# Kernel optimization log

Hardware: AMD Instinct MI355X
Metric: run time of the kernel (lower is better)

The kernel has to match this reference:

```python
import jax, jax.numpy as jnp
import numpy as np

B, FEAT, SPD_H, CTRL_H, N_CMD = 32768, 512, 128, 256, 4


def _p(key, shape, fan_in):
    # torch nn.Linear default init: U(-1/sqrt(fan_in), 1/sqrt(fan_in))
    lim = 1.0 / np.sqrt(fan_in)
    return jax.random.uniform(key, shape, jnp.float32, -lim, lim)


def setup_inputs() -> dict:
    key = jax.random.key(0)
    ks = iter(jax.random.split(key, 32))
    inp = {
        "feat": jax.random.normal(next(ks), (B, FEAT), jnp.float32),
        "speed": jax.random.uniform(next(ks), (B,), jnp.float32),
        "command": jax.random.randint(next(ks), (B,), 0, N_CMD, jnp.int32),
        "ms_w1": _p(next(ks), (1, SPD_H), 1), "ms_b1": _p(next(ks), (SPD_H,), 1),
        "ms_w2": _p(next(ks), (SPD_H, SPD_H), SPD_H), "ms_b2": _p(next(ks), (SPD_H,), SPD_H),
        "ms_w3": _p(next(ks), (SPD_H, SPD_H), SPD_H), "ms_b3": _p(next(ks), (SPD_H,), SPD_H),
        # speed_pred_module: 512 -> 256 -> 256 -> 1
        "sp_w1": _p(next(ks), (FEAT, CTRL_H), FEAT), "sp_b1": _p(next(ks), (CTRL_H,), FEAT),
        "sp_w2": _p(next(ks), (CTRL_H, CTRL_H), CTRL_H), "sp_b2": _p(next(ks), (CTRL_H,), CTRL_H),
        "sp_w3": _p(next(ks), (CTRL_H, 1), CTRL_H), "sp_b3": _p(next(ks), (1,), CTRL_H),
        # join_module: Linear(640, 512)
        "join_w": _p(next(ks), (FEAT + SPD_H, FEAT), FEAT + SPD_H),
        "join_b": _p(next(ks), (FEAT,), FEAT + SPD_H),
        # 4 control heads: 512 -> 256 -> 256 -> 3 (stacked on expert axis e)
        "ctrl_w1": _p(next(ks), (N_CMD, FEAT, CTRL_H), FEAT), "ctrl_b1": _p(next(ks), (N_CMD, CTRL_H), FEAT),
        "ctrl_w2": _p(next(ks), (N_CMD, CTRL_H, CTRL_H), CTRL_H), "ctrl_b2": _p(next(ks), (N_CMD, CTRL_H), CTRL_H),
        "ctrl_w3": _p(next(ks), (N_CMD, CTRL_H, 3), CTRL_H), "ctrl_b3": _p(next(ks), (N_CMD, 3), CTRL_H),
    }
    return inp


def _mlp(x, w1, b1, w2, b2, w3, b3):
    # FullyConnectedNet: Linear, ReLU, Linear, Dropout(p=0 -> noop), ReLU, Linear
    h = jax.nn.relu(x @ w1 + b1)
    h = jax.nn.relu(h @ w2 + b2)
    return h @ w3 + b3


def reference(feat, speed, command,
              ms_w1, ms_b1, ms_w2, ms_b2, ms_w3, ms_b3,
              sp_w1, sp_b1, sp_w2, sp_b2, sp_w3, sp_b3,
              join_w, join_b,
              ctrl_w1, ctrl_b1, ctrl_w2, ctrl_b2, ctrl_w3, ctrl_b3):
    v = _mlp(speed[:, None], ms_w1, ms_b1, ms_w2, ms_b2, ms_w3, ms_b3)      # [B,128]
    joined = jnp.concatenate([feat, v], axis=1) @ join_w + join_b           # [B,512]
    v_p = _mlp(feat, sp_w1, sp_b1, sp_w2, sp_b2, sp_w3, sp_b3)              # [B,1]
    # command-indexed dispatch: compute all 4 heads densely, then select per sample
    h1 = jax.nn.relu(jnp.einsum('bd,edh->beh', joined, ctrl_w1) + ctrl_b1)  # [B,4,256]
    h2 = jax.nn.relu(jnp.einsum('beh,ehk->bek', h1, ctrl_w2) + ctrl_b2)     # [B,4,256]
    act_all = jnp.einsum('bek,eko->beo', h2, ctrl_w3) + ctrl_b3             # [B,4,3]
    action = jnp.take_along_axis(act_all, command[:, None, None].astype(jnp.int32), axis=1)[:, 0]  # [B,3]
    throttle = jax.nn.sigmoid(action[:, 0])
    steering = jnp.tanh(action[:, 1])
    brake = jax.nn.sigmoid(action[:, 2])
    return v_p, throttle, brake, steering
```

## Files before the change

kernel.cpp:

```cpp
#include <hip/hip_runtime.h>
#include <hip/hip_bf16.h>
#include <stdint.h>
#include <math.h>

#define BB 32768
#define FEAT 512
#define SPD_H 128
#define CTRL_H 256
#define NCMD 4

typedef __attribute__((ext_vector_type(8))) short bf16x8;
typedef __attribute__((ext_vector_type(4))) float f32x4;

__device__ __forceinline__ unsigned short f2bf(float f) {
  union { float f; uint32_t u; } v; v.f = f;
  uint32_t u = v.u;
  return (unsigned short)((u + 0x7fffu + ((u >> 16) & 1u)) >> 16);
}

__device__ __forceinline__ void async16(const unsigned short* g, unsigned short* l) {
  __builtin_amdgcn_global_load_lds(
      (const __attribute__((address_space(1))) unsigned int*)g,
      (__attribute__((address_space(3))) unsigned int*)l, 16, 0, 0);
}

__device__ __forceinline__ void gemm128(
    const unsigned short* __restrict__ A, int lda,
    const int* __restrict__ perm, int m_start, int m_cnt,
    const unsigned short* __restrict__ W, const float* __restrict__ bi,
    unsigned short* __restrict__ C, int ldc, int relu, int K, int mt, int nt) {
  extern __shared__ __align__(16) unsigned char dynsm[];
  unsigned short* As = (unsigned short*)dynsm;
  unsigned short* Bs = As + 128 * 32;

  const int m0 = mt * 128;
  if (m0 >= m_cnt) return;
  const int n0 = nt * 128;
  const int t = threadIdx.x;
  const int w = t >> 6, lane = t & 63;
  const int wm = w & 1, wn = w >> 1;

  f32x4 acc[4][4];
#pragma unroll
  for (int i = 0; i < 4; ++i)
#pragma unroll
    for (int j = 0; j < 4; ++j)
#pragma unroll
      for (int r = 0; r < 4; ++r) acc[i][j][r] = 0.f;

  const int fr = lane & 15;
  const int fk = (lane >> 4) * 8;

  const unsigned short* agp[2]; const unsigned short* bgp[2];
  unsigned short* al[2]; unsigned short* bl[2];
#pragma unroll
  for (int it = 0; it < 2; ++it) {
    int row = w * 32 + it * 16 + (lane >> 2);
    int seg8 = (lane & 3) * 8;
    int rl = m0 + row;
    if (rl >= m_cnt) rl = m_cnt - 1;
    int grow = perm ? perm[m_start + rl] : (m_start + rl);
    agp[it] = A + (size_t)grow * lda + seg8;
    bgp[it] = W + (size_t)(n0 + row) * K + seg8;
    al[it] = As + (w * 32 + it * 16) * 32;
    bl[it] = Bs + (w * 32 + it * 16) * 32;
  }

  for (int k0 = 0; k0 < K; k0 += 32) {
#pragma unroll
    for (int it = 0; it < 2; ++it) {
      async16(agp[it] + k0, al[it]);
      async16(bgp[it] + k0, bl[it]);
    }
    __syncthreads();
    bf16x8 af[4], bfv[4];
#pragma unroll
    for (int i = 0; i < 4; ++i)
      af[i] = *(const bf16x8*)(As + (wm * 64 + i * 16 + fr) * 32 + fk);
#pragma unroll
    for (int j = 0; j < 4; ++j)
      bfv[j] = *(const bf16x8*)(Bs + (wn * 64 + j * 16 + fr) * 32 + fk);
#pragma unroll
    for (int i = 0; i < 4; ++i)
#pragma unroll
      for (int j = 0; j < 4; ++j)
        acc[i][j] = __builtin_amdgcn_mfma_f32_16x16x32_bf16(af[i], bfv[j], acc[i][j], 0, 0, 0);
    __syncthreads();
  }

  const int rquad = (lane >> 4) * 4;
  const int cidx = lane & 15;

  float bv[4];
#pragma unroll
  for (int j = 0; j < 4; ++j) bv[j] = bi ? bi[n0 + wn * 64 + j * 16 + cidx] : 0.f;

  unsigned short (*bscr)[136] = (unsigned short(*)[136])dynsm;
#pragma unroll
  for (int c = 0; c < 4; ++c) {
    if (wm == (c >> 1)) {
#pragma unroll
      for (int j = 0; j < 4; ++j) {
#pragma unroll
        for (int ii = 0; ii < 2; ++ii) {
          int i = 2 * (c & 1) + ii;
          int lr = ii * 16 + rquad;
#pragma unroll
          for (int r = 0; r < 4; ++r) {
            float v = acc[i][j][r] + bv[j];
            if (relu) v = fmaxf(v, 0.f);
            bscr[lr + r][wn * 64 + j * 16 + cidx] = f2bf(v);
          }
        }
      }
    }
    __syncthreads();
#pragma unroll
    for (int q = 0; q < 2; ++q) {
      int sg = t + 256 * q;
      int lr = sg >> 4, cs = (sg & 15) * 8;
      int grow = m0 + c * 32 + lr;
      if (grow < m_cnt)
        *(bf16x8*)(C + (size_t)(m_start + grow) * ldc + (n0 + cs)) =
            *(const bf16x8*)(&bscr[lr][cs]);
    }
    __syncthreads();
  }
}

struct WSeg { const float* src; unsigned short* dst; int K; int N; int ldd; };
struct PrepArgs {
  WSeg s[12];
  int start[13];
  const float* join_w; unsigned short* wjbf;
  const float* feat; unsigned short* ajoin;
  const int* cmd; int* wavecnt;
  const float* join_b; const float* ctrl_w1; const float* ctrl_b1; float* b_f;
};
__launch_bounds__(256)
__global__ void k_prep(PrepArgs a) {
  int bx = blockIdx.x, t = threadIdx.x;
  if (bx < 16384) {
    int idx = bx * 256 + t;
    int i = idx >> 7;
    int j4 = (idx & 127) << 2;
    float4 f = *(const float4*)(a.feat + (size_t)i * FEAT + j4);
    ushort4 o;
    o.x = f2bf(f.x); o.y = f2bf(f.y); o.z = f2bf(f.z); o.w = f2bf(f.w);
    *(ushort4*)(a.ajoin + (size_t)i * 640 + j4) = o;
    return;
  }
  int rel = bx - 16384;
  if (rel < 320) {
    int idx = rel * 256 + t;
    float4 f = *(const float4*)(a.join_w + (size_t)idx * 4);
    ushort4 o;
    o.x = f2bf(f.x); o.y = f2bf(f.y); o.z = f2bf(f.z); o.w = f2bf(f.w);
    *(ushort4*)(a.wjbf + (size_t)idx * 4) = o;
    return;
  }
  rel -= 320;
  if (rel < a.start[12]) {
    __shared__ float tb[32][33];
    int si = 0;
    while (rel >= a.start[si + 1]) ++si;
    WSeg sg = a.s[si];
    int tile = rel - a.start[si];
    int tkx = sg.K >> 5;
    int tn = tile / tkx;
    int tk = tile - tn * tkx;
    int k0 = tk * 32, n0 = tn * 32;
    int tx = t & 31, ty = t >> 5;
#pragma unroll
    for (int j = 0; j < 4; ++j)
      tb[ty + j * 8][tx] = sg.src[(size_t)(k0 + ty + j * 8) * sg.N + n0 + tx];
    __syncthreads();
#pragma unroll
    for (int j = 0; j < 4; ++j)
      sg.dst[(size_t)(n0 + ty + j * 8) * sg.ldd + k0 + tx] = f2bf(tb[tx][ty + j * 8]);
    return;
  }
  rel -= a.start[12];
  if (rel < 128) {
    int i = rel * 256 + t;
    int c = a.cmd[i];
    int wid = i >> 6;
    int lane = t & 63;
#pragma unroll
    for (int cv = 0; cv < NCMD; ++cv) {
      unsigned long long m = __ballot(c == cv);
      if (lane == 0) a.wavecnt[cv * 512 + wid] = __popcll(m);
    }
    return;
  }
  int e = rel - 128;
  float s = a.ctrl_b1[e * 256 + t];
  const float* w = a.ctrl_w1 + (size_t)e * 512 * 256 + t;
  for (int m = 0; m < 512; ++m) s = fmaf(a.join_b[m], w[(size_t)m * 256], s);
  a.b_f[e * 256 + t] = s;
}

struct MidArgs {
  const int* cmd; const int* wavecnt; int* perm; int* offs;
  const unsigned short* c_w1t; const unsigned short* wjbf; unsigned short* wf_t;
  const float* speed;
  const float* ms_w1; const float* ms_b1;
  const unsigned short* ms_w2t; const float* ms_b2;
  const unsigned short* ms_w3t; const float* ms_b3;
  unsigned short* ajoin;
};
__launch_bounds__(256)
__global__ void k_mid(MidArgs a) {
  int b = blockIdx.x, t = threadIdx.x;
  if (b >= 168) {
    extern __shared__ __align__(16) unsigned char dynsm[];
    unsigned short (*hw)[136] = (unsigned short(*)[136])dynsm;
    unsigned short* BsM = (unsigned short*)(dynsm + 128 * 136 * 2);
    const int m0 = (b - 168) * 128;
    const int w = t >> 6, lane = t & 63;
    const int wm = w & 1, wn = w >> 1;
    const int fr = lane & 15, fk = (lane >> 4) * 8;
    const int rquad = (lane >> 4) * 4, cidx = lane & 15;
    {
      int r = t >> 1, half = t & 1;
      float s = a.speed[m0 + r];
#pragma unroll
      for (int c0 = 0; c0 < 64; c0 += 4) {
        int c = half * 64 + c0;
        float4 wv = *(const float4*)(a.ms_w1 + c);
        float4 bv = *(const float4*)(a.ms_b1 + c);
        hw[r][c + 0] = f2bf(fmaxf(fmaf(s, wv.x, bv.x), 0.f));
        hw[r][c + 1] = f2bf(fmaxf(fmaf(s, wv.y, bv.y), 0.f));
        hw[r][c + 2] = f2bf(fmaxf(fmaf(s, wv.z, bv.z), 0.f));
        hw[r][c + 3] = f2bf(fmaxf(fmaf(s, wv.w, bv.w), 0.f));
      }
    }
    __syncthreads();
    for (int layer = 0; layer < 2; ++layer) {
      const unsigned short* Wt = layer ? a.ms_w3t : a.ms_w2t;
      const float* bb = layer ? a.ms_b3 : a.ms_b2;
      f32x4 acc[4][4];
#pragma unroll
      for (int i = 0; i < 4; ++i)
#pragma unroll
        for (int j = 0; j < 4; ++j)
#pragma unroll
          for (int r = 0; r < 4; ++r) acc[i][j][r] = 0.f;
      for (int k0 = 0; k0 < 128; k0 += 32) {
#pragma unroll
        for (int it = 0; it < 2; ++it) {
          int row = w * 32 + it * 16 + (lane >> 2);
          async16(Wt + (size_t)row * 128 + k0 + (lane & 3) * 8,
                  BsM + (w * 32 + it * 16) * 32);
        }
        __syncthreads();
        bf16x8 af[4], bfv[4];
#pragma unroll
        for (int i = 0; i < 4; ++i)
          af[i] = *(const bf16x8*)(&hw[wm * 64 + i * 16 + fr][k0 + fk]);
#pragma unroll
        for (int j = 0; j < 4; ++j)
          bfv[j] = *(const bf16x8*)(BsM + (wn * 64 + j * 16 + fr) * 32 + fk);
#pragma unroll
        for (int i = 0; i < 4; ++i)
#pragma unroll
          for (int j = 0; j < 4; ++j)
            acc[i][j] = __builtin_amdgcn_mfma_f32_16x16x32_bf16(af[i], bfv[j], acc[i][j], 0, 0, 0);
        __syncthreads();
      }
#pragma unroll
      for (int j = 0; j < 4; ++j) {
        int col = wn * 64 + j * 16 + cidx;
        float bv = bb[col];
#pragma unroll
        for (int i = 0; i < 4; ++i) {
          int row = wm * 64 + i * 16 + rquad;
#pragma unroll
          for (int r = 0; r < 4; ++r) {
            float v = acc[i][j][r] + bv;
            if (layer == 0) v = fmaxf(v, 0.f);
            hw[row + r][col] = f2bf(v);
          }
        }
      }
      __syncthreads();
    }
    {
      int r = t >> 1, half = t & 1;
#pragma unroll
      for (int c8 = 0; c8 < 8; ++c8)
        *(bf16x8*)(a.ajoin + (size_t)(m0 + r) * 640 + 512 + half * 64 + c8 * 8) =
            *(const bf16x8*)(&hw[r][half * 64 + c8 * 8]);
    }
    return;
  }
  if (b >= 128) {
    int idx = b - 128;
    int mt = idx & 7, nt = idx >> 3;
    gemm128(a.c_w1t, 512, nullptr, 0, 1024, a.wjbf, nullptr, a.wf_t, 640, 0, 512, mt, nt);
    return;
  }
  __shared__ int pf[NCMD][4];
  __shared__ int tot[NCMD];
  int c = t >> 6, lane = t & 63;
  int v[8]; int s = 0;
#pragma unroll
  for (int q = 0; q < 8; ++q) { v[q] = a.wavecnt[c * 512 + lane * 8 + q]; s += v[q]; }
  int p = s;
#pragma unroll
  for (int m = 1; m < 64; m <<= 1) { int o = __shfl_up(p, m, 64); if (lane >= m) p += o; }
  int excl = p - s;
  if (lane == 63) tot[c] = p;
  if (lane == ((4 * b) >> 3)) {
    int base_off = (4 * b) & 7;
    int run = excl;
#pragma unroll
    for (int q = 0; q < 8; ++q) {
      if (q >= base_off && q < base_off + 4) pf[c][q - base_off] = run;
      run += v[q];
    }
  }
  __syncthreads();
  int soffs[NCMD + 1];
  soffs[0] = 0;
#pragma unroll
  for (int e = 0; e < NCMD; ++e) soffs[e + 1] = soffs[e] + tot[e];
  if (b == 0 && t == 0)
    for (int e = 0; e <= NCMD; ++e) a.offs[e] = soffs[e];
  int i = b * 256 + t;
  int mc = a.cmd[i];
  int lwid = t >> 6;
  int rank = 0, base = 0;
#pragma unroll
  for (int cv = 0; cv < NCMD; ++cv) {
    unsigned long long m = __ballot(mc == cv);
    if (mc == cv) {
      rank = __popcll(m & ((1ull << lane) - 1ull));
      base = soffs[cv] + pf[cv][lwid];
    }
  }
  a.perm[base + rank] = i;
}

struct MainArgs {
  const unsigned short* ajoin;
  const unsigned short* wf_t; const float* b_f;
  const unsigned short* sp_w1t; const float* sp_b1;
  unsigned short* ch1; unsigned short* sph1p;
  const int* perm; const int* seg;
};
__launch_bounds__(256)
__global__ void k_main(MainArgs a) {
  const int e = blockIdx.z;
  const int gid = blockIdx.x;
  const int mt = gid & 255, nt = gid >> 8;
  int ms = a.seg[e], mc = a.seg[e + 1] - ms;
  if (nt < 2) {
    gemm128(a.ajoin, 640, a.perm, ms, mc, a.wf_t + (size_t)e * 256 * 640,
            a.b_f + e * 256, a.ch1, 256, 1, 640, mt, nt);
  } else {
    gemm128(a.ajoin, 640, a.perm, ms, mc, a.sp_w1t, a.sp_b1,
            a.sph1p, 256, 1, 512, mt, nt - 2);
  }
}

struct VArgs {
  const unsigned short* A_s; const unsigned short* A_c;
  const unsigned short* W_s; const unsigned short* W_c;
  const float* b_s; const float* b_c;
  const float* w3_s; const float* b3_s;
  const float* w3_c; const float* b3_c;
  const int* perm; const int* seg;
  float* out;
};
__launch_bounds__(256)
__global__ void k_vgemm(VArgs a) {
  __shared__ unsigned short As[64 * 32];
  __shared__ unsigned short Bs[256 * 32];
  const int z = blockIdx.z;
  const unsigned short* A; const unsigned short* W; const float* bi;
  int m_start, m_cnt;
  if (z == 4) { A = a.A_s; W = a.W_s; bi = a.b_s; m_start = 0; m_cnt = BB; }
  else {
    A = a.A_c; W = a.W_c + (size_t)z * 65536; bi = a.b_c + z * 256;
    m_start = a.seg[z]; m_cnt = a.seg[z + 1] - m_start;
  }
  const int m0 = blockIdx.x * 64;
  if (m0 >= m_cnt) return;
  const int t = threadIdx.x, w = t >> 6, lane = t & 63;
  const int fr = lane & 15, fk = (lane >> 4) * 8;

  f32x4 acc[16];
#pragma unroll
  for (int j = 0; j < 16; ++j)
#pragma unroll
    for (int r = 0; r < 4; ++r) acc[j][r] = 0.f;

  int arow = m0 + w * 16 + (lane >> 2);
  if (arow >= m_cnt) arow = m_cnt - 1;
  const unsigned short* ap = A + (size_t)(m_start + arow) * 256 + (lane & 3) * 8;
  unsigned short* al = As + (w * 16) * 32;
  const unsigned short* bp[4]; unsigned short* bl[4];
#pragma unroll
  for (int it = 0; it < 4; ++it) {
    int brow = w * 64 + it * 16 + (lane >> 2);
    bp[it] = W + (size_t)brow * 256 + (lane & 3) * 8;
    bl[it] = Bs + (w * 64 + it * 16) * 32;
  }

  for (int k0 = 0; k0 < 256; k0 += 32) {
    async16(ap + k0, al);
#pragma unroll
    for (int it = 0; it < 4; ++it) async16(bp[it] + k0, bl[it]);
    __syncthreads();
    bf16x8 af = *(const bf16x8*)(As + (w * 16 + fr) * 32 + fk);
#pragma unroll
    for (int j = 0; j < 16; ++j) {
      bf16x8 bfv = *(const bf16x8*)(Bs + (j * 16 + fr) * 32 + fk);
      acc[j] = __builtin_amdgcn_mfma_f32_16x16x32_bf16(af, bfv, acc[j], 0, 0, 0);
    }
    __syncthreads();
  }

  const int rquad = (lane >> 4) * 4;
  float bcol[16];
#pragma unroll
  for (int j = 0; j < 16; ++j) bcol[j] = bi[j * 16 + fr];

  if (z == 4) {
    float aw[16];
#pragma unroll
    for (int j = 0; j < 16; ++j) aw[j] = a.w3_s[j * 16 + fr];
#pragma unroll
    for (int r = 0; r < 4; ++r) {
      float s = 0.f;
#pragma unroll
      for (int j = 0; j < 16; ++j)
        s = fmaf(fmaxf(acc[j][r] + bcol[j], 0.f), aw[j], s);
      s += __shfl_xor(s, 1, 64);
      s += __shfl_xor(s, 2, 64);
      s += __shfl_xor(s, 4, 64);
      s += __shfl_xor(s, 8, 64);
      int row = m0 + w * 16 + rquad + r;
      if (fr == 0 && row < m_cnt)
        a.out[a.perm[row]] = s + a.b3_s[0];
    }
  } else {
    float aw0[16], aw1[16], aw2[16];
#pragma unroll
    for (int j = 0; j < 16; ++j) {
      const float* wp = a.w3_c + (size_t)z * 768 + (j * 16 + fr) * 3;
      aw0[j] = wp[0]; aw1[j] = wp[1]; aw2[j] = wp[2];
    }
#pragma unroll
    for (int r = 0; r < 4; ++r) {
      float s0 = 0.f, s1 = 0.f, s2 = 0.f;
#pragma unroll
      for (int j = 0; j < 16; ++j) {
        float v = fmaxf(acc[j][r] + bcol[j], 0.f);
        s0 = fmaf(v, aw0[j], s0);
        s1 = fmaf(v, aw1[j], s1);
        s2 = fmaf(v, aw2[j], s2);
      }
#pragma unroll
      for (int m = 1; m <= 8; m <<= 1) {
        s0 += __shfl_xor(s0, m, 64);
        s1 += __shfl_xor(s1, m, 64);
        s2 += __shfl_xor(s2, m, 64);
      }
      int row = m0 + w * 16 + rquad + r;
      if (fr == 0 && row < m_cnt) {
        int orig = a.perm[m_start + row];
        float a0 = s0 + a.b3_c[z * 3 + 0];
        float a1 = s1 + a.b3_c[z * 3 + 1];
        float a2 = s2 + a.b3_c[z * 3 + 2];
        a.out[BB + orig]     = 1.f / (1.f + __expf(-a0));
        a.out[2 * BB + orig] = 1.f / (1.f + __expf(-a2));
        a.out[3 * BB + orig] = tanhf(a1);
      }
    }
  }
}

static inline size_t align256(size_t x) { return (x + 255) & ~(size_t)255; }

extern "C" void kernel_launch(void* const* d_in, const int* in_sizes, int n_in,
                              void* d_out, int out_size, void* d_ws, size_t ws_size,
                              hipStream_t stream) {
  const float* feat   = (const float*)d_in[0];
  const float* speed  = (const float*)d_in[1];
  const int*   command= (const int*)d_in[2];
  const float* ms_w1  = (const float*)d_in[3];
  const float* ms_b1  = (const float*)d_in[4];
  const float* ms_w2  = (const float*)d_in[5];
  const float* ms_b2  = (const float*)d_in[6];
  const float* ms_w3  = (const float*)d_in[7];
  const float* ms_b3  = (const float*)d_in[8];
  const float* sp_w1  = (const float*)d_in[9];
  const float* sp_b1  = (const float*)d_in[10];
  const float* sp_w2  = (const float*)d_in[11];
  const float* sp_b2  = (const float*)d_in[12];
  const float* sp_w3  = (const float*)d_in[13];
  const float* sp_b3  = (const float*)d_in[14];
  const float* join_w = (const float*)d_in[15];
  const float* join_b = (const float*)d_in[16];
  const float* ctrl_w1= (const float*)d_in[17];
  const float* ctrl_b1= (const float*)d_in[18];
  const float* ctrl_w2= (const float*)d_in[19];
  const float* ctrl_b2= (const float*)d_in[20];
  const float* ctrl_w3= (const float*)d_in[21];
  const float* ctrl_b3= (const float*)d_in[22];
  float* out = (float*)d_out;

  char* ws = (char*)d_ws;
  size_t off = 0;
  auto alloc = [&](size_t bytes) -> char* { char* p = ws + off; off = align256(off + bytes); return p; };

  unsigned short* ajoin  = (unsigned short*)alloc((size_t)BB * 640 * 2);
  unsigned short* sph1p  = (unsigned short*)alloc((size_t)BB * 256 * 2);
  unsigned short* ch1    = (unsigned short*)alloc((size_t)BB * 256 * 2);
  unsigned short* wtp    = (unsigned short*)alloc(1998848ull * 2);
  int* perm    = (int*)alloc((size_t)BB * 4);
  int* cnt     = (int*)alloc(64);
  int* wavecnt = (int*)alloc(4 * 512 * 4);
  float* b_f   = (float*)alloc(4 * 256 * 4);

  unsigned short* sp_w1t = wtp;
  unsigned short* sp_w2t = wtp + 131072;
  unsigned short* ms_w2t = wtp + 196608;
  unsigned short* ms_w3t = wtp + 212992;
  unsigned short* c_w1t  = wtp + 229376;
  unsigned short* c_w2t  = wtp + 753664;
  unsigned short* wjbf   = wtp + 1015808;
  unsigned short* wf_t   = wtp + 1343488;

  PrepArgs P;
  P.s[0] = { sp_w1, sp_w1t, 512, 256, 512 };
  P.s[1] = { sp_w2, sp_w2t, 256, 256, 256 };
  P.s[2] = { ms_w2, ms_w2t, 128, 128, 128 };
  P.s[3] = { ms_w3, ms_w3t, 128, 128, 128 };
  for (int e = 0; e < 4; ++e) P.s[4 + e] = { ctrl_w1 + (size_t)e * 512 * 256, c_w1t + (size_t)e * 131072, 512, 256, 512 };
  for (int e = 0; e < 4; ++e) P.s[8 + e] = { ctrl_w2 + (size_t)e * 256 * 256, c_w2t + (size_t)e * 65536, 256, 256, 256 };
  P.start[0] = 0;
  for (int i = 0; i < 12; ++i)
    P.start[i + 1] = P.start[i] + (P.s[i].K >> 5) * (P.s[i].N >> 5);
  P.join_w = join_w; P.wjbf = wjbf;
  P.feat = feat; P.ajoin = ajoin;
  P.cmd = command; P.wavecnt = wavecnt;
  P.join_b = join_b; P.ctrl_w1 = ctrl_w1; P.ctrl_b1 = ctrl_b1; P.b_f = b_f;
  int prep_blocks = 16384 + 320 + P.start[12] + 128 + 4;

  k_prep<<<prep_blocks, 256, 0, stream>>>(P);

  MidArgs Mi;
  Mi.cmd = command; Mi.wavecnt = wavecnt; Mi.perm = perm; Mi.offs = cnt + 4;
  Mi.c_w1t = c_w1t; Mi.wjbf = wjbf; Mi.wf_t = wf_t;
  Mi.speed = speed;
  Mi.ms_w1 = ms_w1; Mi.ms_b1 = ms_b1;
  Mi.ms_w2t = ms_w2t; Mi.ms_b2 = ms_b2;
  Mi.ms_w3t = ms_w3t; Mi.ms_b3 = ms_b3;
  Mi.ajoin = ajoin;
  k_mid<<<168 + 256, 256, 128 * 136 * 2 + 128 * 32 * 2, stream>>>(Mi);

  MainArgs Ma;
  Ma.ajoin = ajoin; Ma.wf_t = wf_t; Ma.b_f = b_f;
  Ma.sp_w1t = sp_w1t; Ma.sp_b1 = sp_b1;
  Ma.ch1 = ch1; Ma.sph1p = sph1p;
  Ma.perm = perm; Ma.seg = cnt + 4;
  k_main<<<dim3(1024, 1, 4), 256, 128 * 32 * 2 * 2, stream>>>(Ma);

  VArgs V;
  V.A_s = sph1p; V.A_c = ch1; V.W_s = sp_w2t; V.W_c = c_w2t;
  V.b_s = sp_b2; V.b_c = ctrl_b2;
  V.w3_s = sp_w3; V.b3_s = sp_b3; V.w3_c = ctrl_w3; V.b3_c = ctrl_b3;
  V.perm = perm; V.seg = cnt + 4; V.out = out;
  k_vgemm<<<dim3(512, 1, 5), 256, 0, stream>>>(V);
}
```

Before: 232.8 us.

## Triple-buffer GEMM loads, compact expert tile grid, split bias fold, unpermute speed head

The 128x128 GEMM now uses three LDS stages with asynchronous global-to-LDS prefetch two k-steps ahead and explicit vmcnt waits, and k_vgemm double-buffers its loads. This hides load latency behind the MFMA work. k_main launches a compact list of per-expert 128-row tiles built in k_mid instead of 1024x4 mostly idle blocks, and the speed-prediction GEMM runs on unpermuted rows so its output write no longer goes through perm. The join-bias fold into the ctrl_w1 bias is split across 32 blocks with partial sums that are reduced in k_mid. The cost is more LDS per block (48 KB), which may lower occupancy.

```diff
diff --git a/kernel.cpp b/kernel.cpp
--- a/kernel.cpp
+++ b/kernel.cpp
@@ -24,14 +24,14 @@
       (__attribute__((address_space(3))) unsigned int*)l, 16, 0, 0);
 }
 
-__device__ __forceinline__ void gemm128(
+__device__ __forceinline__ void gemm128_db(
     const unsigned short* __restrict__ A, int lda,
     const int* __restrict__ perm, int m_start, int m_cnt,
     const unsigned short* __restrict__ W, const float* __restrict__ bi,
     unsigned short* __restrict__ C, int ldc, int relu, int K, int mt, int nt) {
   extern __shared__ __align__(16) unsigned char dynsm[];
   unsigned short* As = (unsigned short*)dynsm;
-  unsigned short* Bs = As + 128 * 32;
+  unsigned short* Bs = As + 3 * 4096;
 
   const int m0 = mt * 128;
   if (m0 >= m_cnt) return;
@@ -66,26 +66,49 @@
     bl[it] = Bs + (w * 32 + it * 16) * 32;
   }
 
-  for (int k0 = 0; k0 < K; k0 += 32) {
+  const int nk = K >> 5;
+#pragma unroll
+  for (int it = 0; it < 2; ++it) { async16(agp[it], al[it]); async16(bgp[it], bl[it]); }
+  if (nk > 1) {
 #pragma unroll
     for (int it = 0; it < 2; ++it) {
-      async16(agp[it] + k0, al[it]);
-      async16(bgp[it] + k0, bl[it]);
-    }
-    __syncthreads();
+      async16(agp[it] + 32, al[it] + 4096);
+      async16(bgp[it] + 32, bl[it] + 4096);
+    }
+  }
+
+  int bk = 0;
+  for (int k = 0; k < nk; ++k) {
+    int bn = bk + 2; if (bn >= 3) bn -= 3;
+    if (k + 2 < nk) {
+#pragma unroll
+      for (int it = 0; it < 2; ++it) {
+        async16(agp[it] + (k + 2) * 32, al[it] + bn * 4096);
+        async16(bgp[it] + (k + 2) * 32, bl[it] + bn * 4096);
+      }
+      asm volatile("s_waitcnt vmcnt(8)" ::: "memory");
+    } else if (k + 1 < nk) {
+      asm volatile("s_waitcnt vmcnt(4)" ::: "memory");
+    } else {
+      asm volatile("s_waitcnt vmcnt(0)" ::: "memory");
+    }
+    asm volatile("s_barrier" ::: "memory");
+    const unsigned short* Ab = As + bk * 4096;
+    const unsigned short* Bb = Bs + bk * 4096;
     bf16x8 af[4], bfv[4];
 #pragma unroll
     for (int i = 0; i < 4; ++i)
-      af[i] = *(const bf16x8*)(As + (wm * 64 + i * 16 + fr) * 32 + fk);
+      af[i] = *(const bf16x8*)(Ab + (wm * 64 + i * 16 + fr) * 32 + fk);
 #pragma unroll
     for (int j = 0; j < 4; ++j)
-      bfv[j] = *(const bf16x8*)(Bs + (wn * 64 + j * 16 + fr) * 32 + fk);
+      bfv[j] = *(const bf16x8*)(Bb + (wn * 64 + j * 16 + fr) * 32 + fk);
 #pragma unroll
     for (int i = 0; i < 4; ++i)
 #pragma unroll
       for (int j = 0; j < 4; ++j)
         acc[i][j] = __builtin_amdgcn_mfma_f32_16x16x32_bf16(af[i], bfv[j], acc[i][j], 0, 0, 0);
-    __syncthreads();
+    asm volatile("s_barrier" ::: "memory");
+    ++bk; if (bk == 3) bk = 0;
   }
 
   const int rquad = (lane >> 4) * 4;
@@ -135,7 +158,7 @@
   const float* join_w; unsigned short* wjbf;
   const float* feat; unsigned short* ajoin;
   const int* cmd; int* wavecnt;
-  const float* join_b; const float* ctrl_w1; const float* ctrl_b1; float* b_f;
+  const float* join_b; const float* ctrl_w1; float* bf_part;
 };
 __launch_bounds__(256)
 __global__ void k_prep(PrepArgs a) {
@@ -193,11 +216,25 @@
     }
     return;
   }
-  int e = rel - 128;
-  float s = a.ctrl_b1[e * 256 + t];
-  const float* w = a.ctrl_w1 + (size_t)e * 512 * 256 + t;
-  for (int m = 0; m < 512; ++m) s = fmaf(a.join_b[m], w[(size_t)m * 256], s);
-  a.b_f[e * 256 + t] = s;
+  int idx = rel - 128;
+  int e = idx >> 3, ch = idx & 7;
+  const float* w = a.ctrl_w1 + (size_t)e * 512 * 256 + (size_t)ch * 64 * 256 + t;
+  const float* jb = a.join_b + ch * 64;
+  float s0 = 0.f, s1 = 0.f, s2 = 0.f, s3 = 0.f;
+  float s4 = 0.f, s5 = 0.f, s6 = 0.f, s7 = 0.f;
+#pragma unroll
+  for (int g = 0; g < 8; ++g) {
+    s0 = fmaf(jb[g * 8 + 0], w[(size_t)(g * 8 + 0) * 256], s0);
+    s1 = fmaf(jb[g * 8 + 1], w[(size_t)(g * 8 + 1) * 256], s1);
+    s2 = fmaf(jb[g * 8 + 2], w[(size_t)(g * 8 + 2) * 256], s2);
+    s3 = fmaf(jb[g * 8 + 3], w[(size_t)(g * 8 + 3) * 256], s3);
+    s4 = fmaf(jb[g * 8 + 4], w[(size_t)(g * 8 + 4) * 256], s4);
+    s5 = fmaf(jb[g * 8 + 5], w[(size_t)(g * 8 + 5) * 256], s5);
+    s6 = fmaf(jb[g * 8 + 6], w[(size_t)(g * 8 + 6) * 256], s6);
+    s7 = fmaf(jb[g * 8 + 7], w[(size_t)(g * 8 + 7) * 256], s7);
+  }
+  a.bf_part[(size_t)(e * 8 + ch) * 256 + t] =
+      ((s0 + s1) + (s2 + s3)) + ((s4 + s5) + (s6 + s7));
 }
 
 struct MidArgs {
@@ -208,10 +245,20 @@
   const unsigned short* ms_w2t; const float* ms_b2;
   const unsigned short* ms_w3t; const float* ms_b3;
   unsigned short* ajoin;
+  const float* bf_part; const float* ctrl_b1; float* b_f;
+  int* tile_e; int* tile_r0; int* ntl;
 };
 __launch_bounds__(256)
 __global__ void k_mid(MidArgs a) {
   int b = blockIdx.x, t = threadIdx.x;
+  if (b >= 424) {
+    int e = b - 424;
+    float s = a.ctrl_b1[e * 256 + t];
+#pragma unroll
+    for (int ch = 0; ch < 8; ++ch) s += a.bf_part[(size_t)(e * 8 + ch) * 256 + t];
+    a.b_f[e * 256 + t] = s;
+    return;
+  }
   if (b >= 168) {
     extern __shared__ __align__(16) unsigned char dynsm[];
     unsigned short (*hw)[136] = (unsigned short(*)[136])dynsm;
@@ -297,7 +344,7 @@
   if (b >= 128) {
     int idx = b - 128;
     int mt = idx & 7, nt = idx >> 3;
-    gemm128(a.c_w1t, 512, nullptr, 0, 1024, a.wjbf, nullptr, a.wf_t, 640, 0, 512, mt, nt);
+    gemm128_db(a.c_w1t, 512, nullptr, 0, 1024, a.wjbf, nullptr, a.wf_t, 640, 0, 512, mt, nt);
     return;
   }
   __shared__ int pf[NCMD][4];
@@ -340,27 +387,46 @@
     }
   }
   a.perm[base + rank] = i;
+
+  if (b == 0) {
+    int toff[NCMD + 1];
+    toff[0] = 0;
+#pragma unroll
+    for (int ee = 0; ee < NCMD; ++ee) toff[ee + 1] = toff[ee] + ((tot[ee] + 127) >> 7);
+    if (t == 0) a.ntl[0] = toff[NCMD];
+    for (int ti = t; ti < toff[NCMD]; ti += 256) {
+      int ee = 0;
+      while (ti >= toff[ee + 1]) ++ee;
+      a.tile_e[ti] = ee;
+      a.tile_r0[ti] = soffs[ee] + (ti - toff[ee]) * 128;
+    }
+  }
 }
 
 struct MainArgs {
   const unsigned short* ajoin;
   const unsigned short* wf_t; const float* b_f;
   const unsigned short* sp_w1t; const float* sp_b1;
-  unsigned short* ch1; unsigned short* sph1p;
+  unsigned short* ch1; unsigned short* sph1;
   const int* perm; const int* seg;
+  const int* tile_e; const int* tile_r0; const int* ntl;
 };
 __launch_bounds__(256)
 __global__ void k_main(MainArgs a) {
-  const int e = blockIdx.z;
-  const int gid = blockIdx.x;
-  const int mt = gid & 255, nt = gid >> 8;
-  int ms = a.seg[e], mc = a.seg[e + 1] - ms;
-  if (nt < 2) {
-    gemm128(a.ajoin, 640, a.perm, ms, mc, a.wf_t + (size_t)e * 256 * 640,
-            a.b_f + e * 256, a.ch1, 256, 1, 640, mt, nt);
+  const int z = blockIdx.z;
+  if (z < 2) {
+    int ti = blockIdx.x;
+    if (ti >= a.ntl[0]) return;
+    int e = a.tile_e[ti];
+    int r0 = a.tile_r0[ti];
+    int mc = a.seg[e + 1] - r0; if (mc > 128) mc = 128;
+    gemm128_db(a.ajoin, 640, a.perm, r0, mc, a.wf_t + (size_t)e * 256 * 640,
+               a.b_f + e * 256, a.ch1, 256, 1, 640, 0, z);
   } else {
-    gemm128(a.ajoin, 640, a.perm, ms, mc, a.sp_w1t, a.sp_b1,
-            a.sph1p, 256, 1, 512, mt, nt - 2);
+    int mt = blockIdx.x;
+    if (mt >= 256) return;
+    gemm128_db(a.ajoin, 640, nullptr, 0, BB, a.sp_w1t, a.sp_b1,
+               a.sph1, 256, 1, 512, mt, z - 2);
   }
 }
 
@@ -375,8 +441,8 @@
 };
 __launch_bounds__(256)
 __global__ void k_vgemm(VArgs a) {
-  __shared__ unsigned short As[64 * 32];
-  __shared__ unsigned short Bs[256 * 32];
+  __shared__ unsigned short As[2 * 64 * 32];
+  __shared__ unsigned short Bs[2 * 256 * 32];
   const int z = blockIdx.z;
   const unsigned short* A; const unsigned short* W; const float* bi;
   int m_start, m_cnt;
@@ -408,18 +474,29 @@
     bl[it] = Bs + (w * 64 + it * 16) * 32;
   }
 
-  for (int k0 = 0; k0 < 256; k0 += 32) {
-    async16(ap + k0, al);
-#pragma unroll
-    for (int it = 0; it < 4; ++it) async16(bp[it] + k0, bl[it]);
-    __syncthreads();
-    bf16x8 af = *(const bf16x8*)(As + (w * 16 + fr) * 32 + fk);
+  async16(ap, al);
+#pragma unroll
+  for (int it = 0; it < 4; ++it) async16(bp[it], bl[it]);
+
+  for (int k = 0; k < 8; ++k) {
+    const int cur = (k & 1) * 2048, curB = (k & 1) * 8192;
+    if (k + 1 < 8) {
+      const int nxt = ((k + 1) & 1) * 2048, nxtB = ((k + 1) & 1) * 8192;
+      async16(ap + (k + 1) * 32, al + nxt);
+#pragma unroll
+      for (int it = 0; it < 4; ++it) async16(bp[it] + (k + 1) * 32, bl[it] + nxtB);
+      asm volatile("s_waitcnt vmcnt(5)" ::: "memory");
+    } else {
+      asm volatile("s_waitcnt vmcnt(0)" ::: "memory");
+    }
+    asm volatile("s_barrier" ::: "memory");
+    bf16x8 af = *(const bf16x8*)(As + cur + (w * 16 + fr) * 32 + fk);
 #pragma unroll
     for (int j = 0; j < 16; ++j) {
-      bf16x8 bfv = *(const bf16x8*)(Bs + (j * 16 + fr) * 32 + fk);
+      bf16x8 bfv = *(const bf16x8*)(Bs + curB + (j * 16 + fr) * 32 + fk);
       acc[j] = __builtin_amdgcn_mfma_f32_16x16x32_bf16(af, bfv, acc[j], 0, 0, 0);
     }
-    __syncthreads();
+    asm volatile("s_barrier" ::: "memory");
   }
 
   const int rquad = (lane >> 4) * 4;
@@ -443,7 +520,7 @@
       s += __shfl_xor(s, 8, 64);
       int row = m0 + w * 16 + rquad + r;
       if (fr == 0 && row < m_cnt)
-        a.out[a.perm[row]] = s + a.b3_s[0];
+        a.out[row] = s + a.b3_s[0];
     }
   } else {
     float aw0[16], aw1[16], aw2[16];
@@ -517,13 +594,17 @@
   auto alloc = [&](size_t bytes) -> char* { char* p = ws + off; off = align256(off + bytes); return p; };
 
   unsigned short* ajoin  = (unsigned short*)alloc((size_t)BB * 640 * 2);
-  unsigned short* sph1p  = (unsigned short*)alloc((size_t)BB * 256 * 2);
+  unsigned short* sph1   = (unsigned short*)alloc((size_t)BB * 256 * 2);
   unsigned short* ch1    = (unsigned short*)alloc((size_t)BB * 256 * 2);
   unsigned short* wtp    = (unsigned short*)alloc(1998848ull * 2);
   int* perm    = (int*)alloc((size_t)BB * 4);
   int* cnt     = (int*)alloc(64);
   int* wavecnt = (int*)alloc(4 * 512 * 4);
+  float* bf_part = (float*)alloc(4 * 8 * 256 * 4);
   float* b_f   = (float*)alloc(4 * 256 * 4);
+  int* tile_e  = (int*)alloc(272 * 4);
+  int* tile_r0 = (int*)alloc(272 * 4);
+  int* ntl     = (int*)alloc(64);
 
   unsigned short* sp_w1t = wtp;
   unsigned short* sp_w2t = wtp + 131072;
@@ -547,8 +628,8 @@
   P.join_w = join_w; P.wjbf = wjbf;
   P.feat = feat; P.ajoin = ajoin;
   P.cmd = command; P.wavecnt = wavecnt;
-  P.join_b = join_b; P.ctrl_w1 = ctrl_w1; P.ctrl_b1 = ctrl_b1; P.b_f = b_f;
-  int prep_blocks = 16384 + 320 + P.start[12] + 128 + 4;
+  P.join_b = join_b; P.ctrl_w1 = ctrl_w1; P.bf_part = bf_part;
+  int prep_blocks = 16384 + 320 + P.start[12] + 128 + 32;
 
   k_prep<<<prep_blocks, 256, 0, stream>>>(P);
 
@@ -560,17 +641,20 @@
   Mi.ms_w2t = ms_w2t; Mi.ms_b2 = ms_b2;
   Mi.ms_w3t = ms_w3t; Mi.ms_b3 = ms_b3;
   Mi.ajoin = ajoin;
-  k_mid<<<168 + 256, 256, 128 * 136 * 2 + 128 * 32 * 2, stream>>>(Mi);
+  Mi.bf_part = bf_part; Mi.ctrl_b1 = ctrl_b1; Mi.b_f = b_f;
+  Mi.tile_e = tile_e; Mi.tile_r0 = tile_r0; Mi.ntl = ntl;
+  k_mid<<<168 + 256 + 4, 256, 49152, stream>>>(Mi);
 
   MainArgs Ma;
   Ma.ajoin = ajoin; Ma.wf_t = wf_t; Ma.b_f = b_f;
   Ma.sp_w1t = sp_w1t; Ma.sp_b1 = sp_b1;
-  Ma.ch1 = ch1; Ma.sph1p = sph1p;
+  Ma.ch1 = ch1; Ma.sph1 = sph1;
   Ma.perm = perm; Ma.seg = cnt + 4;
-  k_main<<<dim3(1024, 1, 4), 256, 128 * 32 * 2 * 2, stream>>>(Ma);
+  Ma.tile_e = tile_e; Ma.tile_r0 = tile_r0; Ma.ntl = ntl;
+  k_main<<<dim3(260, 1, 4), 256, 49152, stream>>>(Ma);
 
   VArgs V;
-  V.A_s = sph1p; V.A_c = ch1; V.W_s = sp_w2t; V.W_c = c_w2t;
+  V.A_s = sph1; V.A_c = ch1; V.W_s = sp_w2t; V.W_c = c_w2t;
   V.b_s = sp_b2; V.b_c = ctrl_b2;
   V.w3_s = sp_w3; V.b3_s = sp_b3; V.w3_c = ctrl_w3; V.b3_c = ctrl_b3;
   V.perm = perm; V.seg = cnt + 4; V.out = out;
```

New measurement: 223.2 us. -4.1%, faster.
